# Kernel tuning notes

Hardware: AMD Instinct MI355X
Metric: run time of the kernel (lower is better)

Reference implementation:

```python
import jax, jax.numpy as jnp
import numpy as np


def _maxpool2x2(x):
    # x: [B, C, H, W] -> [B, C, H//2, W//2]
    B, C, H, W = x.shape
    return x.reshape(B, C, H // 2, 2, W // 2, 2).max(axis=(3, 5))


def setup_inputs() -> dict:
    key = jax.random.key(0)
    ks = jax.random.split(key, 6)
    B, CH, H, W = 16, 128, 64, 64
    W_SCALE = 0.05  # keep pre-softmax logits in a sane range
    x = jax.random.normal(ks[0], (B, CH, H, W), dtype=jnp.float32)
    w_theta = jax.random.normal(ks[1], (CH // 8, CH), dtype=jnp.float32) * W_SCALE
    w_phi = jax.random.normal(ks[2], (CH // 8, CH), dtype=jnp.float32) * W_SCALE
    w_g = jax.random.normal(ks[3], (CH // 2, CH), dtype=jnp.float32) * W_SCALE
    w_o = jax.random.normal(ks[4], (CH, CH // 2), dtype=jnp.float32) * W_SCALE
    gamma = jax.random.normal(ks[5], (1,), dtype=jnp.float32)  # torch inits to 0; randomized for non-trivial output
    return {"x": x, "w_theta": w_theta, "w_phi": w_phi, "w_g": w_g, "w_o": w_o, "gamma": gamma}


def reference(x, w_theta, w_phi, w_g, w_o, gamma):
    B, C, H, W = x.shape
    N = H * W
    # 1x1 convs are channel GEMMs
    theta = jnp.einsum('oc,bchw->bohw', w_theta, x)          # [B, C/8, H, W]
    phi = _maxpool2x2(jnp.einsum('oc,bchw->bohw', w_phi, x))  # [B, C/8, H/2, W/2]
    g = _maxpool2x2(jnp.einsum('oc,bchw->bohw', w_g, x))      # [B, C/2, H/2, W/2]
    theta = theta.reshape(B, C // 8, N)        # [B, C/8, N]
    phi = phi.reshape(B, C // 8, N // 4)       # [B, C/8, N/4]
    g = g.reshape(B, C // 2, N // 4)           # [B, C/2, N/4]
    scores = jnp.einsum('bcn,bcm->bnm', theta, phi)  # [B, N, N/4]
    beta = jax.nn.softmax(scores, axis=-1)
    o = jnp.einsum('bcm,bnm->bcn', g, beta)          # [B, C/2, N]
    o = o.reshape(B, C // 2, H, W)
    o = jnp.einsum('oc,bchw->bohw', w_o, o)          # [B, C, H, W]
    return gamma[0] * o + x
```

## Files before the change

### kernel.cpp

```cpp
#include <hip/hip_runtime.h>


typedef __attribute__((ext_vector_type(8))) short bf16x8;
typedef __attribute__((ext_vector_type(16))) float f32x16;

__device__ __forceinline__ ushort f2bf(float f) {
    uint u = __float_as_uint(f);
    u += 0x7FFFu + ((u >> 16) & 1u);
    return (ushort)(u >> 16);
}
__device__ __forceinline__ uint pk2(float a, float b) {
    return (uint)f2bf(a) | ((uint)f2bf(b) << 16);
}

__global__ __launch_bounds__(256) void k_convs(const float* __restrict__ x,
                                               const float* __restrict__ w_theta,
                                               const float* __restrict__ w_phi,
                                               const float* __restrict__ w_g,
                                               ushort* __restrict__ theta_b,
                                               ushort* __restrict__ phi_b,
                                               ushort* __restrict__ g_b) {
    const int tid = threadIdx.x;
    const bool gpart = blockIdx.x >= 256;
    const int pb = blockIdx.x & 255;
    const int gq = pb * 64 + (tid >> 2);
    const int sub = tid & 3;
    const int b = gq >> 10, m = gq & 1023;
    const int h2 = m >> 5, w2 = m & 31;
    const int n = (2 * h2 + (sub >> 1)) * 64 + 2 * w2 + (sub & 1);
    const float* xp = x + (size_t)b * 128 * 4096 + n;

    if (!gpart) {
        __shared__ float wt[128][32];
        for (int i = tid; i < 2048; i += 256) { int o = i >> 7, c = i & 127; wt[c][o] = w_theta[i]; }
        for (int i = tid; i < 2048; i += 256) { int o = i >> 7, c = i & 127; wt[c][16 + o] = w_phi[i]; }
        __syncthreads();
        float th[16], ph[16];
#pragma unroll
        for (int o = 0; o < 16; ++o) { th[o] = 0.f; ph[o] = 0.f; }
        for (int c = 0; c < 128; ++c) {
            float xv = xp[(size_t)c * 4096];
            const float* wr = wt[c];
#pragma unroll
            for (int o = 0; o < 16; ++o) th[o] = fmaf(wr[o], xv, th[o]);
#pragma unroll
            for (int o = 0; o < 16; ++o) ph[o] = fmaf(wr[16 + o], xv, ph[o]);
        }
        uint4 t0, t1;
        t0.x = pk2(th[0], th[1]);  t0.y = pk2(th[2], th[3]);
        t0.z = pk2(th[4], th[5]);  t0.w = pk2(th[6], th[7]);
        t1.x = pk2(th[8], th[9]);  t1.y = pk2(th[10], th[11]);
        t1.z = pk2(th[12], th[13]); t1.w = pk2(th[14], th[15]);
        uint4* tp = (uint4*)(theta_b + ((size_t)b * 4096 + n) * 16);
        tp[0] = t0; tp[1] = t1;
#pragma unroll
        for (int o = 0; o < 16; ++o) {
            ph[o] = fmaxf(ph[o], __shfl_xor(ph[o], 1));
            ph[o] = fmaxf(ph[o], __shfl_xor(ph[o], 2));
        }
        if (sub == 0) {
            uint4 p0, p1;
            p0.x = pk2(ph[0], ph[1]);  p0.y = pk2(ph[2], ph[3]);
            p0.z = pk2(ph[4], ph[5]);  p0.w = pk2(ph[6], ph[7]);
            p1.x = pk2(ph[8], ph[9]);  p1.y = pk2(ph[10], ph[11]);
            p1.z = pk2(ph[12], ph[13]); p1.w = pk2(ph[14], ph[15]);
            uint4* pp = (uint4*)(phi_b + ((size_t)b * 1024 + m) * 16);
            pp[0] = p0; pp[1] = p1;
        }
    } else {
        __shared__ float wg[128][64];
        __shared__ ushort gt[64][68];
        for (int i = tid; i < 8192; i += 256) { int o = i >> 7, c = i & 127; wg[c][o] = w_g[i]; }
        __syncthreads();
        float gg[64];
#pragma unroll
        for (int o = 0; o < 64; ++o) gg[o] = 0.f;
        for (int c = 0; c < 128; ++c) {
            float xv = xp[(size_t)c * 4096];
            const float* wr = wg[c];
#pragma unroll
            for (int o = 0; o < 64; ++o) gg[o] = fmaf(wr[o], xv, gg[o]);
        }
#pragma unroll
        for (int o = 0; o < 64; ++o) {
            gg[o] = fmaxf(gg[o], __shfl_xor(gg[o], 1));
            gg[o] = fmaxf(gg[o], __shfl_xor(gg[o], 2));
        }
        const int mq = tid >> 2;
        if (sub == 0) {
#pragma unroll
            for (int cc = 0; cc < 16; ++cc) gt[cc][mq] = f2bf(gg[cc]);
        } else if (sub == 1) {
#pragma unroll
            for (int cc = 0; cc < 16; ++cc) gt[16 + cc][mq] = f2bf(gg[16 + cc]);
        } else if (sub == 2) {
#pragma unroll
            for (int cc = 0; cc < 16; ++cc) gt[32 + cc][mq] = f2bf(gg[32 + cc]);
        } else {
#pragma unroll
            for (int cc = 0; cc < 16; ++cc) gt[48 + cc][mq] = f2bf(gg[48 + cc]);
        }
        __syncthreads();
        const int c = tid >> 2, q = tid & 3;
        const uint2* s = (const uint2*)&gt[c][16 * q];
        uint2 v0 = s[0], v1 = s[1], v2 = s[2], v3 = s[3];
        const int bb = pb >> 4, mb = (pb & 15) * 64;
        uint2* dst = (uint2*)(g_b + ((size_t)bb * 64 + c) * 1024 + mb + 16 * q);
        dst[0] = v0; dst[1] = v1; dst[2] = v2; dst[3] = v3;
    }
}

__global__ __launch_bounds__(256) void k_attn(const ushort* __restrict__ theta_b,
                                              const ushort* __restrict__ phi_b,
                                              const ushort* __restrict__ g_b,
                                              const float* __restrict__ w_o,
                                              const float* __restrict__ x,
                                              const float* __restrict__ gamma,
                                              float* __restrict__ out) {
    __shared__ ushort p_t[4][32][68];
    const int tid = threadIdx.x;
    const int wave = tid >> 6, lane = tid & 63;
    const int l31 = lane & 31, h = lane >> 5;
    const int b = blockIdx.x >> 5, nt = blockIdx.x & 31;
    const int n = nt * 128 + wave * 32 + l31;

    bf16x8 thf = *(const bf16x8*)(theta_b + ((size_t)b * 4096 + n) * 16 + h * 8);

    f32x16 o0 = {0,0,0,0,0,0,0,0,0,0,0,0,0,0,0,0};
    f32x16 o1 = {0,0,0,0,0,0,0,0,0,0,0,0,0,0,0,0};
    float sm = 0.f;
    ushort* prow = &p_t[wave][l31][0];

    for (int mt = 0; mt < 32; ++mt) {
        const int m0 = mt * 32;
        bf16x8 phf = *(const bf16x8*)(phi_b + ((size_t)b * 1024 + m0 + l31) * 16 + h * 8);
        f32x16 S = {0,0,0,0,0,0,0,0,0,0,0,0,0,0,0,0};
        S = __builtin_amdgcn_mfma_f32_32x32x16_bf16(phf, thf, S, 0, 0, 0);
        float p[16];
#pragma unroll
        for (int jj = 0; jj < 16; ++jj) { p[jj] = __expf(S[jj]); sm += p[jj]; }
#pragma unroll
        for (int q = 0; q < 4; ++q) {
            uint2 v;
            v.x = pk2(p[4 * q], p[4 * q + 1]);
            v.y = pk2(p[4 * q + 2], p[4 * q + 3]);
            *(uint2*)(prow + 8 * q + 4 * h) = v;
        }
        const ushort* gp = g_b + ((size_t)b * 64 + l31) * 1024 + m0 + 8 * h;
#pragma unroll
        for (int kc = 0; kc < 2; ++kc) {
            uint2 ua = *(const uint2*)(prow + 16 * kc + 8 * h);
            uint2 ub = *(const uint2*)(prow + 16 * kc + 8 * h + 4);
            union { bf16x8 v; uint u[4]; } P;
            P.u[0] = ua.x; P.u[1] = ua.y; P.u[2] = ub.x; P.u[3] = ub.y;
            bf16x8 ga0 = *(const bf16x8*)(gp + 16 * kc);
            bf16x8 ga1 = *(const bf16x8*)(gp + 16 * kc + 32 * 1024);
            o0 = __builtin_amdgcn_mfma_f32_32x32x16_bf16(ga0, P.v, o0, 0, 0, 0);
            o1 = __builtin_amdgcn_mfma_f32_32x32x16_bf16(ga1, P.v, o1, 0, 0, 0);
        }
    }
    sm += __shfl_xor(sm, 32);
    const float inv = 1.f / sm;
#pragma unroll
    for (int jj = 0; jj < 16; ++jj) { o0[jj] *= inv; o1[jj] *= inv; }

    bf16x8 Bf[4];
#pragma unroll
    for (int kc = 0; kc < 4; ++kc) {
        const f32x16& oo = (kc < 2) ? o0 : o1;
        const int base = 8 * (kc & 1);
        uint Pa0 = pk2(oo[base + 0], oo[base + 1]);
        uint Pa1 = pk2(oo[base + 2], oo[base + 3]);
        uint Pb0 = pk2(oo[base + 4], oo[base + 5]);
        uint Pb1 = pk2(oo[base + 6], oo[base + 7]);
        uint z0 = h ? Pa0 : Pb0, z1 = h ? Pa1 : Pb1;
        uint r0 = (uint)__shfl_xor((int)z0, 32);
        uint r1 = (uint)__shfl_xor((int)z1, 32);
        union { bf16x8 v; uint u[4]; } Bx;
        if (h == 0) { Bx.u[0] = Pa0; Bx.u[1] = Pa1; Bx.u[2] = r0;  Bx.u[3] = r1; }
        else        { Bx.u[0] = r0;  Bx.u[1] = r1;  Bx.u[2] = Pb0; Bx.u[3] = Pb1; }
        Bf[kc] = Bx.v;
    }

    const float gm = gamma[0];
#pragma unroll
    for (int cof = 0; cof < 4; ++cof) {
        f32x16 oc = {0,0,0,0,0,0,0,0,0,0,0,0,0,0,0,0};
#pragma unroll
        for (int kc = 0; kc < 4; ++kc) {
            const float* wp = w_o + (32 * cof + l31) * 64 + 16 * kc + 8 * h;
            float4 wa = *(const float4*)(wp);
            float4 wb = *(const float4*)(wp + 4);
            union { bf16x8 v; uint u[4]; } W;
            W.u[0] = pk2(wa.x, wa.y); W.u[1] = pk2(wa.z, wa.w);
            W.u[2] = pk2(wb.x, wb.y); W.u[3] = pk2(wb.z, wb.w);
            oc = __builtin_amdgcn_mfma_f32_32x32x16_bf16(W.v, Bf[kc], oc, 0, 0, 0);
        }
#pragma unroll
        for (int jj = 0; jj < 16; ++jj) {
            int co = 32 * cof + (jj & 3) + 8 * (jj >> 2) + 4 * h;
            size_t idx = ((size_t)(b * 128 + co)) * 4096 + n;
            out[idx] = fmaf(gm, oc[jj], x[idx]);
        }
    }
}

extern "C" void kernel_launch(void* const* d_in, const int* in_sizes, int n_in,
                              void* d_out, int out_size, void* d_ws, size_t ws_size,
                              hipStream_t stream) {
    const float* x       = (const float*)d_in[0];
    const float* w_theta = (const float*)d_in[1];
    const float* w_phi   = (const float*)d_in[2];
    const float* w_g     = (const float*)d_in[3];
    const float* w_o     = (const float*)d_in[4];
    const float* gamma   = (const float*)d_in[5];
    float* out = (float*)d_out;

    ushort* theta_b = (ushort*)d_ws;
    ushort* phi_b   = theta_b + 1048576;
    ushort* g_b     = phi_b + 262144;

    k_convs<<<512, 256, 0, stream>>>(x, w_theta, w_phi, w_g, theta_b, phi_b, g_b);
    k_attn<<<512, 256, 0, stream>>>(theta_b, phi_b, g_b, w_o, x, gamma, out);
}
```

Measured before the change: 171.5 us.

## Prefetch phi/g tiles, shuffle P in registers, fold log2e into theta

The attention loop now loads the next iteration's phi and g fragments before computing the current tile, so global load latency overlaps with the MFMA and exp work. The shared-memory round trip that transposed the probability tile into the B-operand layout is replaced by cross-half-wave shuffles in registers. log2(e) is folded into the theta weights so the loop can use exp2f instead of __expf. The prefetch raises register pressure, and the last iteration issues a wrapped-around redundant load.

```diff
diff --git a/kernel.cpp b/kernel.cpp
--- a/kernel.cpp
+++ b/kernel.cpp
@@ -3,6 +3,8 @@
 
 typedef __attribute__((ext_vector_type(8))) short bf16x8;
 typedef __attribute__((ext_vector_type(16))) float f32x16;
+
+#define LOG2E 1.4426950408889634f
 
 __device__ __forceinline__ ushort f2bf(float f) {
     uint u = __float_as_uint(f);
@@ -32,7 +34,7 @@
 
     if (!gpart) {
         __shared__ float wt[128][32];
-        for (int i = tid; i < 2048; i += 256) { int o = i >> 7, c = i & 127; wt[c][o] = w_theta[i]; }
+        for (int i = tid; i < 2048; i += 256) { int o = i >> 7, c = i & 127; wt[c][o] = w_theta[i] * LOG2E; }
         for (int i = tid; i < 2048; i += 256) { int o = i >> 7, c = i & 127; wt[c][16 + o] = w_phi[i]; }
         __syncthreads();
         float th[16], ph[16];
@@ -117,7 +119,6 @@
                                               const float* __restrict__ x,
                                               const float* __restrict__ gamma,
                                               float* __restrict__ out) {
-    __shared__ ushort p_t[4][32][68];
     const int tid = threadIdx.x;
     const int wave = tid >> 6, lane = tid & 63;
     const int l31 = lane & 31, h = lane >> 5;
@@ -126,39 +127,59 @@
 
     bf16x8 thf = *(const bf16x8*)(theta_b + ((size_t)b * 4096 + n) * 16 + h * 8);
 
+    const ushort* pbase = phi_b + (size_t)b * 1024 * 16 + h * 8;
+    const ushort* gbase = g_b + ((size_t)b * 64 + l31) * 1024 + 8 * h;
+
     f32x16 o0 = {0,0,0,0,0,0,0,0,0,0,0,0,0,0,0,0};
     f32x16 o1 = {0,0,0,0,0,0,0,0,0,0,0,0,0,0,0,0};
-    float sm = 0.f;
-    ushort* prow = &p_t[wave][l31][0];
+    float sm0 = 0.f, sm1 = 0.f;
+
+    bf16x8 phf = *(const bf16x8*)(pbase + (size_t)l31 * 16);
+    bf16x8 gA0 = *(const bf16x8*)(gbase);
+    bf16x8 gA1 = *(const bf16x8*)(gbase + 32 * 1024);
+    bf16x8 gB0 = *(const bf16x8*)(gbase + 16);
+    bf16x8 gB1 = *(const bf16x8*)(gbase + 16 + 32 * 1024);
 
     for (int mt = 0; mt < 32; ++mt) {
-        const int m0 = mt * 32;
-        bf16x8 phf = *(const bf16x8*)(phi_b + ((size_t)b * 1024 + m0 + l31) * 16 + h * 8);
+        const int m1 = ((mt + 1) & 31) * 32;
+        bf16x8 nphf = *(const bf16x8*)(pbase + (size_t)(m1 + l31) * 16);
+        bf16x8 ngA0 = *(const bf16x8*)(gbase + m1);
+        bf16x8 ngA1 = *(const bf16x8*)(gbase + m1 + 32 * 1024);
+        bf16x8 ngB0 = *(const bf16x8*)(gbase + m1 + 16);
+        bf16x8 ngB1 = *(const bf16x8*)(gbase + m1 + 16 + 32 * 1024);
+
         f32x16 S = {0,0,0,0,0,0,0,0,0,0,0,0,0,0,0,0};
         S = __builtin_amdgcn_mfma_f32_32x32x16_bf16(phf, thf, S, 0, 0, 0);
         float p[16];
 #pragma unroll
-        for (int jj = 0; jj < 16; ++jj) { p[jj] = __expf(S[jj]); sm += p[jj]; }
-#pragma unroll
-        for (int q = 0; q < 4; ++q) {
-            uint2 v;
-            v.x = pk2(p[4 * q], p[4 * q + 1]);
-            v.y = pk2(p[4 * q + 2], p[4 * q + 3]);
-            *(uint2*)(prow + 8 * q + 4 * h) = v;
-        }
-        const ushort* gp = g_b + ((size_t)b * 64 + l31) * 1024 + m0 + 8 * h;
-#pragma unroll
-        for (int kc = 0; kc < 2; ++kc) {
-            uint2 ua = *(const uint2*)(prow + 16 * kc + 8 * h);
-            uint2 ub = *(const uint2*)(prow + 16 * kc + 8 * h + 4);
-            union { bf16x8 v; uint u[4]; } P;
-            P.u[0] = ua.x; P.u[1] = ua.y; P.u[2] = ub.x; P.u[3] = ub.y;
-            bf16x8 ga0 = *(const bf16x8*)(gp + 16 * kc);
-            bf16x8 ga1 = *(const bf16x8*)(gp + 16 * kc + 32 * 1024);
-            o0 = __builtin_amdgcn_mfma_f32_32x32x16_bf16(ga0, P.v, o0, 0, 0, 0);
-            o1 = __builtin_amdgcn_mfma_f32_32x32x16_bf16(ga1, P.v, o1, 0, 0, 0);
-        }
-    }
+        for (int jj = 0; jj < 16; ++jj) p[jj] = exp2f(S[jj]);
+        sm0 += ((p[0] + p[1]) + (p[2] + p[3])) + ((p[4] + p[5]) + (p[6] + p[7]));
+        sm1 += ((p[8] + p[9]) + (p[10] + p[11])) + ((p[12] + p[13]) + (p[14] + p[15]));
+
+        uint c0 = pk2(p[0], p[1]),   c1 = pk2(p[2], p[3]);
+        uint c2 = pk2(p[4], p[5]),   c3 = pk2(p[6], p[7]);
+        uint c4 = pk2(p[8], p[9]),   c5 = pk2(p[10], p[11]);
+        uint c6 = pk2(p[12], p[13]), c7 = pk2(p[14], p[15]);
+        uint q0 = (uint)__shfl_xor((int)(h ? c0 : c2), 32);
+        uint q1 = (uint)__shfl_xor((int)(h ? c1 : c3), 32);
+        uint q2 = (uint)__shfl_xor((int)(h ? c4 : c6), 32);
+        uint q3 = (uint)__shfl_xor((int)(h ? c5 : c7), 32);
+        union { bf16x8 v; uint u[4]; } B0, B1;
+        if (h == 0) {
+            B0.u[0] = c0; B0.u[1] = c1; B0.u[2] = q0; B0.u[3] = q1;
+            B1.u[0] = c4; B1.u[1] = c5; B1.u[2] = q2; B1.u[3] = q3;
+        } else {
+            B0.u[0] = q0; B0.u[1] = q1; B0.u[2] = c2; B0.u[3] = c3;
+            B1.u[0] = q2; B1.u[1] = q3; B1.u[2] = c6; B1.u[3] = c7;
+        }
+        o0 = __builtin_amdgcn_mfma_f32_32x32x16_bf16(gA0, B0.v, o0, 0, 0, 0);
+        o1 = __builtin_amdgcn_mfma_f32_32x32x16_bf16(gA1, B0.v, o1, 0, 0, 0);
+        o0 = __builtin_amdgcn_mfma_f32_32x32x16_bf16(gB0, B1.v, o0, 0, 0, 0);
+        o1 = __builtin_amdgcn_mfma_f32_32x32x16_bf16(gB1, B1.v, o1, 0, 0, 0);
+
+        phf = nphf; gA0 = ngA0; gA1 = ngA1; gB0 = ngB0; gB1 = ngB1;
+    }
+    float sm = sm0 + sm1;
     sm += __shfl_xor(sm, 32);
     const float inv = 1.f / sm;
 #pragma unroll
```

Result: faster. 167.9 us (-2.1%).
